# Optimization experiments

Hardware: AMD Instinct MI355X
Metric: run time of the kernel (lower is better)

The kernel has to match this reference:

```python
import jax, jax.numpy as jnp
import numpy as np

N_BINS = 15


def setup_inputs() -> dict:
    key = jax.random.key(0)
    k1, k2 = jax.random.split(key)
    N = 33554432  # 32Mi elements
    logits = jax.random.normal(k1, (N,), dtype=jnp.float32) * 2.0
    labels = jax.random.randint(k2, (N,), 0, 2, dtype=jnp.int32)
    return {"logits": logits, "labels": labels}


def reference(logits, labels):
    # probs = sigmoid(logits); acc = (probs > 0.5) == labels
    probs = jax.nn.sigmoid(logits)
    acc = ((probs > 0.5).astype(labels.dtype) == labels).astype(probs.dtype)

    # Bins are (lower, upper] with edges = linspace(0, 1, n_bins+1).
    # digitize(..., right=True) gives i s.t. edges[i-1] < p <= edges[i].
    edges = jnp.linspace(0.0, 1.0, N_BINS + 1)
    idx = jnp.clip(jnp.digitize(probs, edges, right=True) - 1, 0, N_BINS - 1)
    # p == 0 falls in no bin in the original loop (first bin is (0, 1/15]).
    valid = (probs > edges[0]).astype(probs.dtype)

    # ece = sum_b |mean_conf_b - mean_acc_b| * (count_b / N)
    #     = sum_b |sum_conf_b - sum_acc_b| / N   (empty bins contribute 0)
    sum_conf = jax.ops.segment_sum(probs * valid, idx, num_segments=N_BINS)
    sum_acc = jax.ops.segment_sum(acc * valid, idx, num_segments=N_BINS)
    n = jnp.asarray(probs.size, probs.dtype)
    ece = jnp.sum(jnp.abs(sum_conf - sum_acc)) / n
    return ece.reshape(1)
```

## Files before the change

kernel.cpp:

```cpp
#include <hip/hip_runtime.h>

#define NBINS 15
#define NTHREADS 256
#define NWAVES 4
#define NBLOCKS 2048
#define UNROLL 4

__global__ __launch_bounds__(NTHREADS) void ece_partial_kernel(
    const float* __restrict__ logits,
    const int* __restrict__ labels,
    float* __restrict__ partials,
    int n)
{
    const float CE[NBINS] = { -88.72284f,
        -2.63905733f, -1.87180218f, -1.38629436f, -1.01160091f,
        -0.69314718f, -0.40546511f, -0.13353139f,  0.13353139f,
         0.40546511f,  0.69314718f,  1.01160091f,  1.38629436f,
         1.87180218f,  2.63905733f };

    float S[NBINS];
    #pragma unroll
    for (int k = 0; k < NBINS; ++k) S[k] = 0.0f;

    const int tid  = threadIdx.x;
    const int lane = tid & 63;
    const int w    = tid >> 6;

    const int n4 = n >> 2;
    const float4* L4 = (const float4*)logits;
    const int4*   Y4 = (const int4*)labels;

    const int macroStride = NBLOCKS * NTHREADS * UNROLL;
    const int nMacro = n4 / macroStride;

    int i = blockIdx.x * (NTHREADS * UNROLL) + tid;
    for (int m = 0; m < nMacro; ++m, i += macroStride) {
        float4 x[UNROLL];
        int4   y[UNROLL];
        #pragma unroll
        for (int u = 0; u < UNROLL; ++u) {
            x[u] = L4[i + u * NTHREADS];
            y[u] = Y4[i + u * NTHREADS];
        }
        #pragma unroll
        for (int u = 0; u < UNROLL; ++u) {
            #pragma unroll
            for (int j = 0; j < 4; ++j) {
                float xv = (&x[u].x)[j];
                int   yv = (&y[u].x)[j];
                float p = 1.0f / (1.0f + __expf(-xv));
                float a = ((xv > 0.0f) == (yv != 0)) ? 1.0f : 0.0f;
                float t = p - a;
                #pragma unroll
                for (int k = 0; k < NBINS; ++k)
                    S[k] += (xv > CE[k]) ? t : 0.0f;
            }
        }
    }

    for (int r = nMacro * macroStride + blockIdx.x * NTHREADS + tid;
         r < n4; r += NBLOCKS * NTHREADS) {
        float4 x = L4[r];
        int4   y = Y4[r];
        #pragma unroll
        for (int j = 0; j < 4; ++j) {
            float xv = (&x.x)[j];
            int   yv = (&y.x)[j];
            float p = 1.0f / (1.0f + __expf(-xv));
            float a = ((xv > 0.0f) == (yv != 0)) ? 1.0f : 0.0f;
            float t = p - a;
            #pragma unroll
            for (int k = 0; k < NBINS; ++k)
                S[k] += (xv > CE[k]) ? t : 0.0f;
        }
    }

    if (blockIdx.x == 0) {
        for (int r = (n4 << 2) + tid; r < n; r += NTHREADS) {
            float xv = logits[r];
            int   yv = labels[r];
            float p = 1.0f / (1.0f + __expf(-xv));
            float a = ((xv > 0.0f) == (yv != 0)) ? 1.0f : 0.0f;
            float t = p - a;
            #pragma unroll
            for (int k = 0; k < NBINS; ++k)
                S[k] += (xv > CE[k]) ? t : 0.0f;
        }
    }

    __shared__ float wavesum[NWAVES][NBINS];
    #pragma unroll
    for (int k = 0; k < NBINS; ++k) {
        float s = S[k];
        #pragma unroll
        for (int m2 = 32; m2 >= 1; m2 >>= 1)
            s += __shfl_xor(s, m2, 64);
        if (lane == 0) wavesum[w][k] = s;
    }
    __syncthreads();

    if (tid < NBINS) {
        float s = 0.0f;
        #pragma unroll
        for (int ww = 0; ww < NWAVES; ++ww) s += wavesum[ww][tid];
        partials[blockIdx.x * NBINS + tid] = s;
    }
}

__global__ __launch_bounds__(NTHREADS) void ece_final_kernel(
    const float* __restrict__ partials,
    float* __restrict__ out,
    float inv_n)
{
    __shared__ double red[NBINS];
    const int t = threadIdx.x;
    if (t < 16 * NBINS) {
        const int b   = t >> 4;
        const int sub = t & 15;
        double s = 0.0;
        for (int k = sub; k < NBLOCKS; k += 16)
            s += (double)partials[k * NBINS + b];
        s += __shfl_xor(s, 8, 16);
        s += __shfl_xor(s, 4, 16);
        s += __shfl_xor(s, 2, 16);
        s += __shfl_xor(s, 1, 16);
        if (sub == 0) red[b] = s;
    }
    __syncthreads();
    if (t == 0) {
        double e = 0.0;
        #pragma unroll
        for (int b = 0; b < NBINS - 1; ++b)
            e += fabs(red[b] - red[b + 1]);
        e += fabs(red[NBINS - 1]);
        out[0] = (float)(e * (double)inv_n);
    }
}

extern "C" void kernel_launch(void* const* d_in, const int* in_sizes, int n_in,
                              void* d_out, int out_size, void* d_ws, size_t ws_size,
                              hipStream_t stream)
{
    const float* logits = (const float*)d_in[0];
    const int*   labels = (const int*)d_in[1];
    float* out      = (float*)d_out;
    float* partials = (float*)d_ws;
    const int n = in_sizes[0];

    ece_partial_kernel<<<NBLOCKS, NTHREADS, 0, stream>>>(logits, labels, partials, n);
    ece_final_kernel<<<1, NTHREADS, 0, stream>>>(partials, out, 1.0f / (float)n);
}
```

Before: 97.52 us.

## Assign contiguous per-XCD data chunks to blocks and drop manual unroll

```diff
diff --git a/kernel.cpp b/kernel.cpp
--- a/kernel.cpp
+++ b/kernel.cpp
@@ -4,7 +4,11 @@
 #define NTHREADS 256
 #define NWAVES 4
 #define NBLOCKS 2048
-#define UNROLL 4
+#define TT (NBLOCKS * NTHREADS)
+#define NXCD 8
+
+typedef float f32x4 __attribute__((ext_vector_type(4)));
+typedef int   i32x4 __attribute__((ext_vector_type(4)));
 
 __global__ __launch_bounds__(NTHREADS) void ece_partial_kernel(
     const float* __restrict__ logits,
@@ -25,29 +29,25 @@
     const int tid  = threadIdx.x;
     const int lane = tid & 63;
     const int w    = tid >> 6;
+    const int n4   = n >> 2;
 
-    const int n4 = n >> 2;
-    const float4* L4 = (const float4*)logits;
-    const int4*   Y4 = (const int4*)labels;
+    const f32x4* L4 = (const f32x4*)logits;
+    const i32x4* Y4 = (const i32x4*)labels;
 
-    const int macroStride = NBLOCKS * NTHREADS * UNROLL;
-    const int nMacro = n4 / macroStride;
-
-    int i = blockIdx.x * (NTHREADS * UNROLL) + tid;
-    for (int m = 0; m < nMacro; ++m, i += macroStride) {
-        float4 x[UNROLL];
-        int4   y[UNROLL];
-        #pragma unroll
-        for (int u = 0; u < UNROLL; ++u) {
-            x[u] = L4[i + u * NTHREADS];
-            y[u] = Y4[i + u * NTHREADS];
-        }
-        #pragma unroll
-        for (int u = 0; u < UNROLL; ++u) {
+    if (((n & 3) == 0) && ((n4 & (TT - 1)) == 0)) {
+        const int xcd  = blockIdx.x & (NXCD - 1);
+        const int slot = blockIdx.x >> 3;
+        const int groupsPerXcd   = n4 >> 3;
+        const int groupsPerBlock = n4 / NBLOCKS;
+        const int iters          = groupsPerBlock / NTHREADS;
+        int idx = xcd * groupsPerXcd + slot * groupsPerBlock + tid;
+        for (int m = 0; m < iters; ++m, idx += NTHREADS) {
+            f32x4 x = L4[idx];
+            i32x4 y = Y4[idx];
             #pragma unroll
             for (int j = 0; j < 4; ++j) {
-                float xv = (&x[u].x)[j];
-                int   yv = (&y[u].x)[j];
+                float xv = x[j];
+                int   yv = y[j];
                 float p = 1.0f / (1.0f + __expf(-xv));
                 float a = ((xv > 0.0f) == (yv != 0)) ? 1.0f : 0.0f;
                 float t = p - a;
@@ -56,35 +56,33 @@
                     S[k] += (xv > CE[k]) ? t : 0.0f;
             }
         }
-    }
-
-    for (int r = nMacro * macroStride + blockIdx.x * NTHREADS + tid;
-         r < n4; r += NBLOCKS * NTHREADS) {
-        float4 x = L4[r];
-        int4   y = Y4[r];
-        #pragma unroll
-        for (int j = 0; j < 4; ++j) {
-            float xv = (&x.x)[j];
-            int   yv = (&y.x)[j];
-            float p = 1.0f / (1.0f + __expf(-xv));
-            float a = ((xv > 0.0f) == (yv != 0)) ? 1.0f : 0.0f;
-            float t = p - a;
+    } else {
+        for (int i = blockIdx.x * NTHREADS + tid; i < n4; i += TT) {
+            f32x4 x = L4[i];
+            i32x4 y = Y4[i];
             #pragma unroll
-            for (int k = 0; k < NBINS; ++k)
-                S[k] += (xv > CE[k]) ? t : 0.0f;
+            for (int j = 0; j < 4; ++j) {
+                float xv = x[j];
+                int   yv = y[j];
+                float p = 1.0f / (1.0f + __expf(-xv));
+                float a = ((xv > 0.0f) == (yv != 0)) ? 1.0f : 0.0f;
+                float t = p - a;
+                #pragma unroll
+                for (int k = 0; k < NBINS; ++k)
+                    S[k] += (xv > CE[k]) ? t : 0.0f;
+            }
         }
-    }
-
-    if (blockIdx.x == 0) {
-        for (int r = (n4 << 2) + tid; r < n; r += NTHREADS) {
-            float xv = logits[r];
-            int   yv = labels[r];
-            float p = 1.0f / (1.0f + __expf(-xv));
-            float a = ((xv > 0.0f) == (yv != 0)) ? 1.0f : 0.0f;
-            float t = p - a;
-            #pragma unroll
-            for (int k = 0; k < NBINS; ++k)
-                S[k] += (xv > CE[k]) ? t : 0.0f;
+        if (blockIdx.x == 0) {
+            for (int r = (n4 << 2) + tid; r < n; r += NTHREADS) {
+                float xv = logits[r];
+                int   yv = labels[r];
+                float p = 1.0f / (1.0f + __expf(-xv));
+                float a = ((xv > 0.0f) == (yv != 0)) ? 1.0f : 0.0f;
+                float t = p - a;
+                #pragma unroll
+                for (int k = 0; k < NBINS; ++k)
+                    S[k] += (xv > CE[k]) ? t : 0.0f;
+            }
         }
     }
 
```

After: 97.13 us. No clear change (-0.4%).
